# Kernel optimization log

Hardware: AMD Instinct MI355X
Metric: run time of the kernel (lower is better)

Reference implementation:

```python
import jax, jax.numpy as jnp
import numpy as np
import math

EMBED_DIM = 1024
NUM_HEADS = 4
HEAD_DIM = EMBED_DIM // NUM_HEADS
B, N = 4, 2048


def setup_inputs() -> dict:
    key = jax.random.key(0)
    ks = jax.random.split(key, 5)
    s = 1.0 / math.sqrt(EMBED_DIM)
    return {
        "x": jax.random.normal(ks[0], (B, N, EMBED_DIM), dtype=jnp.float32),
        "w_qkv": jax.random.normal(ks[1], (EMBED_DIM, 3 * EMBED_DIM), dtype=jnp.float32) * s,
        "b_qkv": jnp.zeros((3 * EMBED_DIM,), dtype=jnp.float32),
        "w_out": jax.random.normal(ks[2], (EMBED_DIM, EMBED_DIM), dtype=jnp.float32) * s,
        "b_out": jnp.zeros((EMBED_DIM,), dtype=jnp.float32),
        "ln_gamma": jnp.ones((EMBED_DIM,), dtype=jnp.float32),
        "ln_beta": jnp.zeros((EMBED_DIM,), dtype=jnp.float32),
    }


def reference(x, w_qkv, b_qkv, w_out, b_out, ln_gamma, ln_beta):
    Bx, Nx, D = x.shape
    qkv = x @ w_qkv + b_qkv  # [B, N, 3D]
    q, k, v = jnp.split(qkv, 3, axis=-1)
    # [B, H, N, hd]
    def heads(t):
        return t.reshape(Bx, Nx, NUM_HEADS, HEAD_DIM).transpose(0, 2, 1, 3)
    q, k, v = heads(q), heads(k), heads(v)
    scale = 1.0 / math.sqrt(HEAD_DIM)
    attn = jnp.einsum("bhqd,bhkd->bhqk", q, k) * scale  # [B, H, N, N]
    attn = jax.nn.softmax(attn, axis=-1)
    out = jnp.einsum("bhqk,bhkd->bhqd", attn, v)  # [B, H, N, hd]
    out = out.transpose(0, 2, 1, 3).reshape(Bx, Nx, D)
    out = out @ w_out + b_out
    # residual + LayerNorm (eps=1e-5 like torch default)
    y = x + out
    mu = jnp.mean(y, axis=-1, keepdims=True)
    var = jnp.mean(jnp.square(y - mu), axis=-1, keepdims=True)
    y = (y - mu) * jax.lax.rsqrt(var + 1e-5)
    return y * ln_gamma + ln_beta
```

## Files before the change

kernel.cpp:

```cpp
#include <hip/hip_runtime.h>
#include <hip/hip_bf16.h>

typedef __attribute__((ext_vector_type(8))) short short8;
typedef __attribute__((ext_vector_type(4))) float f32x4;
typedef __attribute__((ext_vector_type(16))) float f32x16;
typedef __attribute__((ext_vector_type(4))) unsigned uint4v;

#define GLOB_AS __attribute__((address_space(1)))
#define LDS_AS  __attribute__((address_space(3)))

__device__ __forceinline__ void async16(void* lds, const void* g) {
  __builtin_amdgcn_global_load_lds((const GLOB_AS unsigned int*)g,
                                   (LDS_AS unsigned int*)lds, 16, 0, 0);
}

__device__ __forceinline__ unsigned short f2bf(float f) {
  unsigned u = __float_as_uint(f);
  unsigned r = u + 0x7FFFu + ((u >> 16) & 1u);
  return (unsigned short)(r >> 16);
}

__device__ __forceinline__ unsigned pk2(float lo, float hi) {
  __hip_bfloat162 h = __float22bfloat162_rn(float2{lo, hi});
  return *reinterpret_cast<unsigned*>(&h);
}

__device__ __forceinline__ void lane32_swap(unsigned& a, unsigned& b, int lane) {
#if __has_builtin(__builtin_amdgcn_permlane32_swap)
  auto r = __builtin_amdgcn_permlane32_swap(a, b, false, false);
  a = r[0]; b = r[1];
#else
  unsigned tb = __shfl_xor(b, 32);
  unsigned ta = __shfl_xor(a, 32);
  unsigned na = (lane < 32) ? a : tb;
  unsigned nb = (lane < 32) ? ta : b;
  a = na; b = nb;
#endif
}

#define BATCH 4
#define SEQ   2048
#define DMODEL 1024
#define NHEAD 4
#define HD    256

#define QSCALE 0.090169944f
#define DEFER_THR 11.5f

__global__ __launch_bounds__(256) void cast_bf16_kernel(
    const float* __restrict__ in, unsigned short* __restrict__ out) {
  int i = blockIdx.x * 256 + threadIdx.x;
  float4 v = ((const float4*)in)[i];
  uint2 o;
  o.x = (unsigned)f2bf(v.x) | ((unsigned)f2bf(v.y) << 16);
  o.y = (unsigned)f2bf(v.z) | ((unsigned)f2bf(v.w) << 16);
  ((uint2*)out)[i] = o;
}

__global__ __launch_bounds__(256) void transpose_cast_kernel(
    const float* __restrict__ in, unsigned short* __restrict__ out, int R, int C) {
  __shared__ float tile[32][33];
  int c0 = blockIdx.x * 32, r0 = blockIdx.y * 32;
  int tx = threadIdx.x, ty = threadIdx.y;
#pragma unroll
  for (int i = 0; i < 4; ++i)
    tile[ty + 8 * i][tx] = in[(size_t)(r0 + ty + 8 * i) * C + c0 + tx];
  __syncthreads();
#pragma unroll
  for (int i = 0; i < 4; ++i)
    out[(size_t)(c0 + ty + 8 * i) * R + r0 + tx] = f2bf(tile[tx][ty + 8 * i]);
}

__global__ __launch_bounds__(256) void gemm_qkv_kernel(
    const unsigned short* __restrict__ A,
    const unsigned short* __restrict__ Bt,
    const float* __restrict__ bias,
    unsigned short* __restrict__ qb,
    unsigned short* __restrict__ kb,
    unsigned short* __restrict__ vt) {
  __shared__ __align__(16) unsigned short sA[128 * 32];
  __shared__ __align__(16) unsigned short sB[128 * 32];
  const int t = threadIdx.x;
  const int l = t & 63, w = t >> 6;
  const int g = l >> 4, lr = l & 15;
  const int wr = w >> 1, wc = w & 1;
  const int row0 = blockIdx.y * 128;
  const int col0 = blockIdx.x * 128;

  f32x4 acc[4][4] = {};
  for (int kt = 0; kt < 1024; kt += 32) {
    __syncthreads();
#pragma unroll
    for (int i = 0; i < 2; ++i) {
      int e = i * 256 + t;
      async16(&sA[e * 8], A + (size_t)(row0 + (e >> 2)) * 1024 + kt + (e & 3) * 8);
      async16(&sB[e * 8], Bt + (size_t)(col0 + (e >> 2)) * 1024 + kt + (e & 3) * 8);
    }
    __syncthreads();
    short8 af[4], bf[4];
#pragma unroll
    for (int m = 0; m < 4; ++m)
      af[m] = *(const short8*)&sA[(wr * 64 + m * 16 + lr) * 32 + g * 8];
#pragma unroll
    for (int n = 0; n < 4; ++n)
      bf[n] = *(const short8*)&sB[(wc * 64 + n * 16 + lr) * 32 + g * 8];
#pragma unroll
    for (int m = 0; m < 4; ++m)
#pragma unroll
      for (int n = 0; n < 4; ++n)
        acc[m][n] = __builtin_amdgcn_mfma_f32_16x16x32_bf16(af[m], bf[n], acc[m][n], 0, 0, 0);
  }

#pragma unroll
  for (int m = 0; m < 4; ++m) {
    int rowb = row0 + wr * 64 + m * 16 + g * 4;
    int b = rowb >> 11;
    int nb = rowb & 2047;
#pragma unroll
    for (int nn = 0; nn < 4; ++nn) {
      int col = col0 + wc * 64 + nn * 16 + lr;
      float bv = bias[col];
      int sec = col >> 10, c1 = col & 1023;
      int h = c1 >> 8, d = c1 & 255;
      if (sec == 2) {
        unsigned short p0 = f2bf(acc[m][nn][0] + bv);
        unsigned short p1 = f2bf(acc[m][nn][1] + bv);
        unsigned short p2 = f2bf(acc[m][nn][2] + bv);
        unsigned short p3 = f2bf(acc[m][nn][3] + bv);
        uint2 pk;
        pk.x = (unsigned)p0 | ((unsigned)p1 << 16);
        pk.y = (unsigned)p2 | ((unsigned)p3 << 16);
        size_t idx = (((size_t)((b * NHEAD + h) * 128 + (nb >> 4))) * 256 + d) * 16 + (nb & 15);
        *(uint2*)&vt[idx] = pk;
      } else {
        unsigned short* dst = (sec == 0) ? qb : kb;
        float sc = (sec == 0) ? QSCALE : 1.0f;
#pragma unroll
        for (int rr = 0; rr < 4; ++rr) {
          size_t idx = ((size_t)((b * NHEAD + h) * SEQ + nb + rr)) * HD + d;
          dst[idx] = f2bf((acc[m][nn][rr] + bv) * sc);
        }
      }
    }
  }
}

__global__ __launch_bounds__(256, 1) void attn_kernel(
    const unsigned short* __restrict__ qb,
    const unsigned short* __restrict__ kb,
    const unsigned short* __restrict__ vt,
    unsigned short* __restrict__ ao) {
  __shared__ __align__(16) unsigned short sK[2][32 * 256];
  const int t = threadIdx.x, l = t & 63, w = t >> 6;
  const int row = l & 31, hi = l >> 5;
  const int swz = (row & 7) << 4;
  const int bid = blockIdx.x;
  const int bh = (bid & 7) * 2 + ((bid >> 3) & 1);
  const int qblk = bid >> 4;
  const int b = bh >> 2, h = bh & 3;
  const int q = qblk * 128 + w * 32 + row;
  const unsigned short* Qp = qb + (size_t)bh * SEQ * HD;
  const char* Kg = (const char*)(kb + (size_t)bh * SEQ * HD);
  const unsigned short* Vb = vt + (size_t)bh * (128 * 256 * 16);

  short8 qf[16];
#pragma unroll
  for (int dc = 0; dc < 16; ++dc)
    qf[dc] = *(const short8*)&Qp[(size_t)q * HD + dc * 16 + hi * 8];

  auto stage = [&](int buf, int kp0) {
#pragma unroll
    for (int i = 0; i < 4; ++i) {
      int s = i * 256 + t;
      int r = s >> 5;
      int colb = (s & 31) * 16;
      int src = (kp0 + r) * 512 + (colb ^ ((r & 7) << 4));
      async16((char*)sK[buf] + s * 16, Kg + src);
    }
  };

  stage(0, 0);
  __syncthreads();

  f32x16 O[8] = {};
  float mrun = -__builtin_inff();
  float lsum = 0.f;

  for (int it = 0; it < 64; ++it) {
    const int kp0 = it * 32;
    const int cur = it & 1;
    if (it < 63) stage(cur ^ 1, kp0 + 32);

    short8 vfr[8][2];
#pragma unroll
    for (int db = 0; db < 8; ++db)
#pragma unroll
      for (int kh = 0; kh < 2; ++kh)
        vfr[db][kh] = *(const short8*)&Vb[(((size_t)((kp0 >> 4) + kh)) * 256 +
                                           db * 32 + row) * 16 + hi * 8];

    f32x16 S = {};
    const char* sKc = (const char*)sK[cur];
#pragma unroll
    for (int dc = 0; dc < 16; ++dc) {
      short8 kf = *(const short8*)(sKc + row * 512 + ((dc * 32 + hi * 16) ^ swz));
      S = __builtin_amdgcn_mfma_f32_32x32x16_bf16(kf, qf[dc], S, 0, 0, 0);
    }

    float p[16];
#pragma unroll
    for (int i = 0; i < 16; ++i) p[i] = S[i];
    float m0 = fmaxf(fmaxf(fmaxf(p[0], p[1]), fmaxf(p[2], p[3])),
                     fmaxf(fmaxf(p[4], p[5]), fmaxf(p[6], p[7])));
    float m1 = fmaxf(fmaxf(fmaxf(p[8], p[9]), fmaxf(p[10], p[11])),
                     fmaxf(fmaxf(p[12], p[13]), fmaxf(p[14], p[15])));
    float cmax = fmaxf(m0, m1);
    cmax = fmaxf(cmax, __shfl_xor(cmax, 32));

    if (!__all(cmax <= mrun + DEFER_THR)) {
      float mnew = fmaxf(mrun, cmax);
      float alpha = exp2f(mrun - mnew);
      lsum *= alpha;
#pragma unroll
      for (int db = 0; db < 8; ++db) O[db] *= alpha;
      mrun = mnew;
    }

    float e[16];
#pragma unroll
    for (int i = 0; i < 16; ++i) e[i] = exp2f(p[i] - mrun);
    float s0 = (e[0] + e[1]) + (e[2] + e[3]);
    float s1 = (e[4] + e[5]) + (e[6] + e[7]);
    float s2 = (e[8] + e[9]) + (e[10] + e[11]);
    float s3 = (e[12] + e[13]) + (e[14] + e[15]);
    float ps = (s0 + s1) + (s2 + s3);
    ps += __shfl_xor(ps, 32);
    lsum += ps;

    unsigned a0 = pk2(e[0], e[1]),   a1 = pk2(e[2], e[3]);
    unsigned b0 = pk2(e[4], e[5]),   b1 = pk2(e[6], e[7]);
    unsigned c0 = pk2(e[8], e[9]),   c1 = pk2(e[10], e[11]);
    unsigned d0 = pk2(e[12], e[13]), d1 = pk2(e[14], e[15]);
    lane32_swap(a0, b0, l);
    lane32_swap(a1, b1, l);
    lane32_swap(c0, d0, l);
    lane32_swap(c1, d1, l);
    uint4v u1; u1.x = a0; u1.y = a1; u1.z = b0; u1.w = b1;
    uint4v u2; u2.x = c0; u2.y = c1; u2.z = d0; u2.w = d1;
    short8 pf1 = __builtin_bit_cast(short8, u1);
    short8 pf2 = __builtin_bit_cast(short8, u2);

#pragma unroll
    for (int db = 0; db < 8; ++db) {
      O[db] = __builtin_amdgcn_mfma_f32_32x32x16_bf16(vfr[db][0], pf1, O[db], 0, 0, 0);
      O[db] = __builtin_amdgcn_mfma_f32_32x32x16_bf16(vfr[db][1], pf2, O[db], 0, 0, 0);
    }

    __syncthreads();
  }

  float inv = 1.0f / lsum;
  size_t obase = ((size_t)(b * SEQ + q)) * DMODEL + h * HD;
#pragma unroll
  for (int db = 0; db < 8; ++db)
#pragma unroll
    for (int rg = 0; rg < 4; ++rg) {
      int dd = db * 32 + rg * 8 + hi * 4;
      uint2 pk;
      pk.x = pk2(O[db][rg * 4 + 0] * inv, O[db][rg * 4 + 1] * inv);
      pk.y = pk2(O[db][rg * 4 + 2] * inv, O[db][rg * 4 + 3] * inv);
      *(uint2*)&ao[obase + dd] = pk;
    }
}

__global__ __launch_bounds__(256) void gemm_out_kernel(
    const unsigned short* __restrict__ A,
    const unsigned short* __restrict__ Bt,
    const float* __restrict__ bias,
    const float* __restrict__ x,
    float* __restrict__ y) {
  __shared__ __align__(16) unsigned short sA[128 * 32];
  __shared__ __align__(16) unsigned short sB[128 * 32];
  const int t = threadIdx.x;
  const int l = t & 63, w = t >> 6;
  const int g = l >> 4, lr = l & 15;
  const int wr = w >> 1, wc = w & 1;
  const int row0 = blockIdx.y * 128;
  const int col0 = blockIdx.x * 128;

  f32x4 acc[4][4] = {};
  for (int kt = 0; kt < 1024; kt += 32) {
    __syncthreads();
#pragma unroll
    for (int i = 0; i < 2; ++i) {
      int e = i * 256 + t;
      async16(&sA[e * 8], A + (size_t)(row0 + (e >> 2)) * 1024 + kt + (e & 3) * 8);
      async16(&sB[e * 8], Bt + (size_t)(col0 + (e >> 2)) * 1024 + kt + (e & 3) * 8);
    }
    __syncthreads();
    short8 af[4], bf[4];
#pragma unroll
    for (int m = 0; m < 4; ++m)
      af[m] = *(const short8*)&sA[(wr * 64 + m * 16 + lr) * 32 + g * 8];
#pragma unroll
    for (int n = 0; n < 4; ++n)
      bf[n] = *(const short8*)&sB[(wc * 64 + n * 16 + lr) * 32 + g * 8];
#pragma unroll
    for (int m = 0; m < 4; ++m)
#pragma unroll
      for (int n = 0; n < 4; ++n)
        acc[m][n] = __builtin_amdgcn_mfma_f32_16x16x32_bf16(af[m], bf[n], acc[m][n], 0, 0, 0);
  }

#pragma unroll
  for (int m = 0; m < 4; ++m) {
    int rowb = row0 + wr * 64 + m * 16 + g * 4;
#pragma unroll
    for (int nn = 0; nn < 4; ++nn) {
      int col = col0 + wc * 64 + nn * 16 + lr;
      float bv = bias[col];
#pragma unroll
      for (int rr = 0; rr < 4; ++rr) {
        size_t idx = (size_t)(rowb + rr) * 1024 + col;
        y[idx] = acc[m][nn][rr] + bv + x[idx];
      }
    }
  }
}

__global__ __launch_bounds__(256) void ln_kernel(
    const float* __restrict__ y, const float* __restrict__ gamma,
    const float* __restrict__ beta, float* __restrict__ out) {
  int row = blockIdx.x, t = threadIdx.x;
  float4 v = ((const float4*)(y + (size_t)row * 1024))[t];
  float s = v.x + v.y + v.z + v.w;
  float qs = v.x * v.x + v.y * v.y + v.z * v.z + v.w * v.w;
#pragma unroll
  for (int off = 1; off < 64; off <<= 1) {
    s += __shfl_xor(s, off);
    qs += __shfl_xor(qs, off);
  }
  __shared__ float ss[4], qq[4];
  if ((t & 63) == 0) { ss[t >> 6] = s; qq[t >> 6] = qs; }
  __syncthreads();
  s = ss[0] + ss[1] + ss[2] + ss[3];
  qs = qq[0] + qq[1] + qq[2] + qq[3];
  float mean = s * (1.0f / 1024.0f);
  float var = qs * (1.0f / 1024.0f) - mean * mean;
  float rstd = rsqrtf(var + 1e-5f);
  float4 gm = ((const float4*)gamma)[t];
  float4 bt = ((const float4*)beta)[t];
  float4 o;
  o.x = (v.x - mean) * rstd * gm.x + bt.x;
  o.y = (v.y - mean) * rstd * gm.y + bt.y;
  o.z = (v.z - mean) * rstd * gm.z + bt.z;
  o.w = (v.w - mean) * rstd * gm.w + bt.w;
  ((float4*)(out + (size_t)row * 1024))[t] = o;
}

extern "C" void kernel_launch(void* const* d_in, const int* in_sizes, int n_in,
                              void* d_out, int out_size, void* d_ws, size_t ws_size,
                              hipStream_t stream) {
  const float* x      = (const float*)d_in[0];
  const float* w_qkv  = (const float*)d_in[1];
  const float* b_qkv  = (const float*)d_in[2];
  const float* w_out  = (const float*)d_in[3];
  const float* b_out  = (const float*)d_in[4];
  const float* gamma  = (const float*)d_in[5];
  const float* beta   = (const float*)d_in[6];
  float* out = (float*)d_out;

  char* ws = (char*)d_ws;
  unsigned short* xb    = (unsigned short*)(ws);
  unsigned short* wqkvT = (unsigned short*)(ws + (16u << 20));
  unsigned short* woutT = (unsigned short*)(ws + (22u << 20));
  unsigned short* qb    = (unsigned short*)(ws + (24u << 20));
  unsigned short* kb    = (unsigned short*)(ws + (40u << 20));
  unsigned short* vt    = (unsigned short*)(ws + (56u << 20));
  unsigned short* ao    = (unsigned short*)(ws + (72u << 20));
  float* y              = (float*)(ws + (88u << 20));

  cast_bf16_kernel<<<(BATCH * SEQ * DMODEL) / (256 * 4), 256, 0, stream>>>(x, xb);
  transpose_cast_kernel<<<dim3(96, 32), dim3(32, 8), 0, stream>>>(w_qkv, wqkvT, 1024, 3072);
  transpose_cast_kernel<<<dim3(32, 32), dim3(32, 8), 0, stream>>>(w_out, woutT, 1024, 1024);
  gemm_qkv_kernel<<<dim3(24, 64), 256, 0, stream>>>(xb, wqkvT, b_qkv, qb, kb, vt);
  attn_kernel<<<256, 256, 0, stream>>>(qb, kb, vt, ao);
  gemm_out_kernel<<<dim3(8, 64), 256, 0, stream>>>(ao, woutT, b_out, x, y);
  ln_kernel<<<BATCH * SEQ, 256, 0, stream>>>(y, gamma, beta, out);
}
```

Baseline: 284.9 us.

## Split attention KV range across two blocks and merge partial softmax results

The attention kernel now runs over half of the key sequence per block. This doubles the grid to 512 blocks with up to two resident blocks per CU, raising occupancy and latency hiding compared with one wave per SIMD. Each half writes a bf16 normalized partial output plus per-row (max, sum) stats, and a new combine kernel merges them with log-sum-exp weights before the output GEMM. The QK accumulation is also split into two independent MFMA chains for more ILP. The cost is an extra kernel launch and roughly 48 MB of extra memory traffic, plus a small extra bf16 rounding on the partial outputs.

Measured after the change: 450.1 us. 58.0% more time.

```diff
diff --git a/kernel.cpp b/kernel.cpp
--- a/kernel.cpp
+++ b/kernel.cpp
@@ -18,6 +18,11 @@
   unsigned u = __float_as_uint(f);
   unsigned r = u + 0x7FFFu + ((u >> 16) & 1u);
   return (unsigned short)(r >> 16);
+}
+
+__device__ __forceinline__ float bf2f(unsigned short u) {
+  unsigned x = ((unsigned)u) << 16;
+  return __uint_as_float(x);
 }
 
 __device__ __forceinline__ unsigned pk2(float lo, float hi) {
@@ -145,18 +150,20 @@
   }
 }
 
-__global__ __launch_bounds__(256, 1) void attn_kernel(
+__global__ __launch_bounds__(256, 2) void attn_kernel(
     const unsigned short* __restrict__ qb,
     const unsigned short* __restrict__ kb,
     const unsigned short* __restrict__ vt,
-    unsigned short* __restrict__ ao) {
+    unsigned short* __restrict__ Oh,
+    float2* __restrict__ st) {
   __shared__ __align__(16) unsigned short sK[2][32 * 256];
   const int t = threadIdx.x, l = t & 63, w = t >> 6;
   const int row = l & 31, hi = l >> 5;
   const int swz = (row & 7) << 4;
   const int bid = blockIdx.x;
   const int bh = (bid & 7) * 2 + ((bid >> 3) & 1);
-  const int qblk = bid >> 4;
+  const int qblk = (bid >> 4) & 15;
+  const int kvhalf = bid >> 8;
   const int b = bh >> 2, h = bh & 3;
   const int q = qblk * 128 + w * 32 + row;
   const unsigned short* Qp = qb + (size_t)bh * SEQ * HD;
@@ -179,17 +186,18 @@
     }
   };
 
-  stage(0, 0);
+  const int kpbase = kvhalf * 1024;
+  stage(0, kpbase);
   __syncthreads();
 
   f32x16 O[8] = {};
   float mrun = -__builtin_inff();
   float lsum = 0.f;
 
-  for (int it = 0; it < 64; ++it) {
-    const int kp0 = it * 32;
+  for (int it = 0; it < 32; ++it) {
+    const int kp0 = kpbase + it * 32;
     const int cur = it & 1;
-    if (it < 63) stage(cur ^ 1, kp0 + 32);
+    if (it < 31) stage(cur ^ 1, kp0 + 32);
 
     short8 vfr[8][2];
 #pragma unroll
@@ -199,17 +207,19 @@
         vfr[db][kh] = *(const short8*)&Vb[(((size_t)((kp0 >> 4) + kh)) * 256 +
                                            db * 32 + row) * 16 + hi * 8];
 
-    f32x16 S = {};
+    f32x16 Sa = {}, Sb = {};
     const char* sKc = (const char*)sK[cur];
 #pragma unroll
-    for (int dc = 0; dc < 16; ++dc) {
-      short8 kf = *(const short8*)(sKc + row * 512 + ((dc * 32 + hi * 16) ^ swz));
-      S = __builtin_amdgcn_mfma_f32_32x32x16_bf16(kf, qf[dc], S, 0, 0, 0);
+    for (int dc = 0; dc < 16; dc += 2) {
+      short8 kf0 = *(const short8*)(sKc + row * 512 + ((dc * 32 + hi * 16) ^ swz));
+      short8 kf1 = *(const short8*)(sKc + row * 512 + (((dc + 1) * 32 + hi * 16) ^ swz));
+      Sa = __builtin_amdgcn_mfma_f32_32x32x16_bf16(kf0, qf[dc], Sa, 0, 0, 0);
+      Sb = __builtin_amdgcn_mfma_f32_32x32x16_bf16(kf1, qf[dc + 1], Sb, 0, 0, 0);
     }
 
     float p[16];
 #pragma unroll
-    for (int i = 0; i < 16; ++i) p[i] = S[i];
+    for (int i = 0; i < 16; ++i) p[i] = Sa[i] + Sb[i];
     float m0 = fmaxf(fmaxf(fmaxf(p[0], p[1]), fmaxf(p[2], p[3])),
                      fmaxf(fmaxf(p[4], p[5]), fmaxf(p[6], p[7])));
     float m1 = fmaxf(fmaxf(fmaxf(p[8], p[9]), fmaxf(p[10], p[11])),
@@ -260,6 +270,7 @@
   }
 
   float inv = 1.0f / lsum;
+  unsigned short* aop = Oh + (size_t)kvhalf * (8192ull * 1024);
   size_t obase = ((size_t)(b * SEQ + q)) * DMODEL + h * HD;
 #pragma unroll
   for (int db = 0; db < 8; ++db)
@@ -269,8 +280,41 @@
       uint2 pk;
       pk.x = pk2(O[db][rg * 4 + 0] * inv, O[db][rg * 4 + 1] * inv);
       pk.y = pk2(O[db][rg * 4 + 2] * inv, O[db][rg * 4 + 3] * inv);
-      *(uint2*)&ao[obase + dd] = pk;
-    }
+      *(uint2*)&aop[obase + dd] = pk;
+    }
+  if (hi == 0)
+    st[((size_t)kvhalf * 16 + bh) * 2048 + q] = make_float2(mrun, lsum);
+}
+
+__global__ __launch_bounds__(256) void combine_kernel(
+    const unsigned short* __restrict__ Oh,
+    const float2* __restrict__ st,
+    unsigned short* __restrict__ ao) {
+  int rowg = blockIdx.x, t = threadIdx.x;
+  int b = rowg >> 11, q = rowg & 2047;
+  int col = t * 4;
+  int bh = b * 4 + (col >> 8);
+  float2 s0 = st[(size_t)bh * 2048 + q];
+  float2 s1 = st[(16ull * 2048) + (size_t)bh * 2048 + q];
+  float M = fmaxf(s0.x, s1.x);
+  float w0 = s0.y * exp2f(s0.x - M);
+  float w1 = s1.y * exp2f(s1.x - M);
+  float inv = 1.0f / (w0 + w1);
+  w0 *= inv; w1 *= inv;
+  size_t base = (size_t)rowg * 1024 + col;
+  uint2 ua = *(const uint2*)&Oh[base];
+  uint2 ub = *(const uint2*)&Oh[8192ull * 1024 + base];
+  unsigned short oa[4] = {(unsigned short)(ua.x & 0xFFFF), (unsigned short)(ua.x >> 16),
+                          (unsigned short)(ua.y & 0xFFFF), (unsigned short)(ua.y >> 16)};
+  unsigned short ob[4] = {(unsigned short)(ub.x & 0xFFFF), (unsigned short)(ub.x >> 16),
+                          (unsigned short)(ub.y & 0xFFFF), (unsigned short)(ub.y >> 16)};
+  float r[4];
+#pragma unroll
+  for (int j = 0; j < 4; ++j) r[j] = w0 * bf2f(oa[j]) + w1 * bf2f(ob[j]);
+  uint2 pk;
+  pk.x = pk2(r[0], r[1]);
+  pk.y = pk2(r[2], r[3]);
+  *(uint2*)&ao[base] = pk;
 }
 
 __global__ __launch_bounds__(256) void gemm_out_kernel(
@@ -378,13 +422,16 @@
   unsigned short* kb    = (unsigned short*)(ws + (40u << 20));
   unsigned short* vt    = (unsigned short*)(ws + (56u << 20));
   unsigned short* ao    = (unsigned short*)(ws + (72u << 20));
+  unsigned short* Oh    = (unsigned short*)(ws + (88u << 20));
   float* y              = (float*)(ws + (88u << 20));
+  float2* st            = (float2*)(ws + (16u << 20));
 
   cast_bf16_kernel<<<(BATCH * SEQ * DMODEL) / (256 * 4), 256, 0, stream>>>(x, xb);
   transpose_cast_kernel<<<dim3(96, 32), dim3(32, 8), 0, stream>>>(w_qkv, wqkvT, 1024, 3072);
   transpose_cast_kernel<<<dim3(32, 32), dim3(32, 8), 0, stream>>>(w_out, woutT, 1024, 1024);
   gemm_qkv_kernel<<<dim3(24, 64), 256, 0, stream>>>(xb, wqkvT, b_qkv, qb, kb, vt);
-  attn_kernel<<<256, 256, 0, stream>>>(qb, kb, vt, ao);
+  attn_kernel<<<512, 256, 0, stream>>>(qb, kb, vt, Oh, st);
+  combine_kernel<<<BATCH * SEQ, 256, 0, stream>>>(Oh, st, ao);
   gemm_out_kernel<<<dim3(8, 64), 256, 0, stream>>>(ao, woutT, b_out, x, y);
   ln_kernel<<<BATCH * SEQ, 256, 0, stream>>>(y, gamma, beta, out);
 }
```
